# Kernel tuning notes

Measured on AMD Instinct MI355X. Metric: run time of the kernel, lower is better.

## Reference

```python
import jax, jax.numpy as jnp
import numpy as np

N = 50000       # nodes
E = 800000      # directed edges (before self-loops)
F_IN = 128      # dataset.num_features
HID = 16        # hidden per head (layer 1)
HEADS = 8
CLASSES = 16    # dataset.num_classes
NEG_SLOPE = 0.2 # GATConv default LeakyReLU slope


def setup_inputs() -> dict:
    key = jax.random.key(0)
    ks = jax.random.split(key, 10)
    s = 0.1  # glorot-ish scale for weights
    x = jax.random.normal(ks[0], (N, F_IN), jnp.float32)
    edge_index = jax.random.randint(ks[1], (2, E), 0, N, jnp.int32)
    W1 = jax.random.normal(ks[2], (F_IN, HEADS * HID), jnp.float32) * s
    a_src1 = jax.random.normal(ks[3], (HEADS, HID), jnp.float32) * s
    a_dst1 = jax.random.normal(ks[4], (HEADS, HID), jnp.float32) * s
    b1 = jnp.zeros((HEADS * HID,), jnp.float32)
    W2 = jax.random.normal(ks[5], (HEADS * HID, CLASSES), jnp.float32) * s
    a_src2 = jax.random.normal(ks[6], (1, CLASSES), jnp.float32) * s
    a_dst2 = jax.random.normal(ks[7], (1, CLASSES), jnp.float32) * s
    b2 = jnp.zeros((CLASSES,), jnp.float32)
    return {"x": x, "edge_index": edge_index, "W1": W1, "a_src1": a_src1,
            "a_dst1": a_dst1, "b1": b1, "W2": W2, "a_src2": a_src2,
            "a_dst2": a_dst2, "b2": b2}


def gat_conv(x, src, dst, W, a_s, a_d, b, concat):
    """PyG GATConv (eval mode): linear -> per-edge LeakyReLU attention ->
    per-destination segment softmax -> scatter-add aggregation."""
    n = x.shape[0]
    H, C = a_s.shape
    h = (x @ W).reshape(n, H, C)                       # [N,H,C]
    alpha_src = jnp.einsum('nhc,hc->nh', h, a_s)       # [N,H]
    alpha_dst = jnp.einsum('nhc,hc->nh', h, a_d)
    e = jax.nn.leaky_relu(alpha_src[src] + alpha_dst[dst], NEG_SLOPE)  # [E,H]
    # numerically stable segment softmax over incoming edges of each dst node
    emax = jax.ops.segment_max(e, dst, num_segments=n)
    emax = jnp.where(jnp.isfinite(emax), emax, 0.0)
    ex = jnp.exp(e - emax[dst])
    denom = jax.ops.segment_sum(ex, dst, num_segments=n)
    alpha = ex / (denom[dst] + 1e-16)                  # [E,H]
    out = jax.ops.segment_sum(alpha[:, :, None] * h[src], dst, num_segments=n)
    out = out.reshape(n, H * C) if concat else out.mean(axis=1)
    return out + b


def reference(x, edge_index, W1, a_src1, a_dst1, b1, W2, a_src2, a_dst2, b2):
    n = x.shape[0]
    loop = jnp.arange(n, dtype=edge_index.dtype)       # GATConv add_self_loops=True
    src = jnp.concatenate([edge_index[0], loop])
    dst = jnp.concatenate([edge_index[1], loop])
    # dropout layers are identity in eval mode
    h = jax.nn.elu(gat_conv(x, src, dst, W1, a_src1, a_dst1, b1, concat=True))
    out = gat_conv(h, src, dst, W2, a_src2, a_dst2, b2, concat=False)
    return out
```

## Files before the change

kernel.cpp:

```cpp
#include <hip/hip_runtime.h>
#include <hip/hip_bf16.h>
#include <math.h>

#define NN 50000
#define NE 800000
#define NBK 196
#define BCAP 5120
#define CHUNK 8192
#define NCH ((NE + CHUNK - 1) / CHUNK)
#define APITCH 136

typedef short bf16x8 __attribute__((ext_vector_type(8)));
typedef float f32x4  __attribute__((ext_vector_type(4)));
typedef float f32x2  __attribute__((ext_vector_type(2)));

__device__ __forceinline__ unsigned short f2bf(float f) {
    union { float f; unsigned int i; } v; v.f = f;
    unsigned int x = v.i;
    unsigned int r = (x >> 16) & 1u;
    x += 0x7fffu + r;
    return (unsigned short)(x >> 16);
}
__device__ __forceinline__ void un2(unsigned int u, float& a, float& b) {
    union { unsigned int i; float f; } x, y;
    x.i = u << 16; y.i = u & 0xffff0000u;
    a = x.f; b = y.f;
}
__device__ __forceinline__ f32x2 up2(unsigned int u) {
    union { unsigned int i; float f; } x, y;
    x.i = u << 16; y.i = u & 0xffff0000u;
    return (f32x2){x.f, y.f};
}

__global__ __launch_bounds__(256) void k_bin(const int* __restrict__ ei,
                                             int* __restrict__ gcur,
                                             unsigned int* __restrict__ packed) {
    __shared__ int h[NBK];
    __shared__ int bas[NBK];
    int t = threadIdx.x;
    if (t < NBK) h[t] = 0;
    __syncthreads();
    int cb = blockIdx.x * CHUNK;
#pragma unroll
    for (int k = 0; k < CHUNK / 256; k++) {
        int i = cb + k * 256 + t;
        if (i < NE) atomicAdd(&h[ei[NE + i] >> 8], 1);
    }
    __syncthreads();
    if (t < NBK) {
        int c = h[t];
        bas[t] = c ? (t * BCAP + atomicAdd(&gcur[t], c)) : 0;
        h[t] = 0;
    }
    __syncthreads();
#pragma unroll
    for (int k = 0; k < CHUNK / 256; k++) {
        int i = cb + k * 256 + t;
        if (i < NE) {
            int s = ei[i], d = ei[NE + i];
            int b = d >> 8;
            int r = atomicAdd(&h[b], 1);
            packed[bas[b] + r] = (unsigned int)s | ((unsigned int)(d & 255) << 16);
        }
    }
}

__global__ __launch_bounds__(256) void k_final(const unsigned int* __restrict__ packed,
                                               const int* __restrict__ gcur,
                                               int* __restrict__ deg,
                                               int* __restrict__ offs,
                                               int* __restrict__ ssrc) {
    __shared__ unsigned int pk[BCAP + 64];
    __shared__ int osl[BCAP + 64];
    __shared__ int cnt[256], pre[256], cur[256];
    int t = threadIdx.x, b = blockIdx.x;
    int start = b * BCAP;
    int n = gcur[b];
    for (int i = t; i < n; i += 256) pk[i] = packed[start + i];
    cnt[t] = 0;
    __syncthreads();
    for (int i = t; i < n; i += 256) atomicAdd(&cnt[(pk[i] >> 16) & 255], 1);
    __syncthreads();
    int v = cnt[t];
    pre[t] = v;
    __syncthreads();
    for (int off = 1; off < 256; off <<= 1) {
        int u = (t >= off) ? pre[t - off] : 0;
        __syncthreads();
        pre[t] += u;
        __syncthreads();
    }
    int excl = pre[t] - v;
    int dst = b * 256 + t;
    if (dst < NN) { deg[dst] = v; offs[dst] = start + excl; }
    cur[t] = excl;
    __syncthreads();
    for (int i = t; i < n; i += 256) {
        unsigned int p = pk[i];
        int r = atomicAdd(&cur[(p >> 16) & 255], 1);
        osl[r] = (int)(p & 0xffffu);
    }
    __syncthreads();
    for (int i = t; i < n; i += 256) ssrc[start + i] = osl[i];
}

__global__ __launch_bounds__(256) void k_swizw(const float* __restrict__ W1,
                                               uint4* __restrict__ W1s) {
    int f = blockIdx.x * 256 + threadIdx.x;
    int nt = f >> 8, kc = (f >> 6) & 3, l = f & 63;
    int n  = nt * 16 + (l & 15);
    int k0 = kc * 32 + (l >> 4) * 8;
    unsigned int p[4];
#pragma unroll
    for (int jj = 0; jj < 4; jj++) {
        float v0 = W1[(k0 + 2 * jj) * 128 + n];
        float v1 = W1[(k0 + 2 * jj + 1) * 128 + n];
        p[jj] = (unsigned int)f2bf(v0) | ((unsigned int)f2bf(v1) << 16);
    }
    W1s[f] = make_uint4(p[0], p[1], p[2], p[3]);
}

__global__ __launch_bounds__(256) void k_gemm1(
    const float* __restrict__ x,
    const uint4* __restrict__ W1s,
    const float* __restrict__ aS,
    const float* __restrict__ aD,
    unsigned short* __restrict__ h1,
    float* __restrict__ as1,
    float* __restrict__ ad1)
{
    __shared__ unsigned short Alds[64 * APITCH];
    int t = threadIdx.x;
    int w = t >> 6, l = t & 63;
    int rowbase = blockIdx.x * 64;

    {
        const float4* xg = (const float4*)(x + (size_t)rowbase * 128);
#pragma unroll
        for (int i = 0; i < 8; i++) {
            int idx = t + 256 * i;
            int r = idx >> 5, c = (idx & 31) * 4;
            float4 v = make_float4(0.f, 0.f, 0.f, 0.f);
            if (rowbase + r < NN) v = xg[idx];
            unsigned int p0 = (unsigned int)f2bf(v.x) | ((unsigned int)f2bf(v.y) << 16);
            unsigned int p1 = (unsigned int)f2bf(v.z) | ((unsigned int)f2bf(v.w) << 16);
            *(uint2*)&Alds[r * APITCH + c] = make_uint2(p0, p1);
        }
    }

    union BU { uint4 u; bf16x8 v; };
    BU b[2][4];
#pragma unroll
    for (int j = 0; j < 2; j++) {
        int nt = 2 * w + j;
#pragma unroll
        for (int kc = 0; kc < 4; kc++)
            b[j][kc].u = W1s[(nt * 4 + kc) * 64 + l];
    }
    __syncthreads();

    f32x4 acc[4][2];
#pragma unroll
    for (int mt = 0; mt < 4; mt++)
#pragma unroll
        for (int j = 0; j < 2; j++) acc[mt][j] = (f32x4){0.f, 0.f, 0.f, 0.f};

    int mrow = l & 15, quad = l >> 4;
#pragma unroll
    for (int kc = 0; kc < 4; kc++) {
#pragma unroll
        for (int mt = 0; mt < 4; mt++) {
            bf16x8 a = *(const bf16x8*)&Alds[(mt * 16 + mrow) * APITCH + kc * 32 + quad * 8];
            acc[mt][0] = __builtin_amdgcn_mfma_f32_16x16x32_bf16(a, b[0][kc].v, acc[mt][0], 0, 0, 0);
            acc[mt][1] = __builtin_amdgcn_mfma_f32_16x16x32_bf16(a, b[1][kc].v, acc[mt][1], 0, 0, 0);
        }
    }

#pragma unroll
    for (int j = 0; j < 2; j++) {
        int head = 2 * w + j;
        float aSv = aS[head * 16 + mrow];
        float aDv = aD[head * 16 + mrow];
#pragma unroll
        for (int mt = 0; mt < 4; mt++) {
#pragma unroll
            for (int reg = 0; reg < 4; reg++) {
                float s = acc[mt][j][reg] * aSv;
                float d = acc[mt][j][reg] * aDv;
                s += __shfl_xor(s, 1); s += __shfl_xor(s, 2);
                s += __shfl_xor(s, 4); s += __shfl_xor(s, 8);
                d += __shfl_xor(d, 1); d += __shfl_xor(d, 2);
                d += __shfl_xor(d, 4); d += __shfl_xor(d, 8);
                if (mrow == 0) {
                    int grow = rowbase + mt * 16 + quad * 4 + reg;
                    if (grow < NN) {
                        as1[grow * 8 + head] = s;
                        ad1[grow * 8 + head] = d;
                    }
                }
            }
        }
    }

    __syncthreads();
#pragma unroll
    for (int mt = 0; mt < 4; mt++)
#pragma unroll
        for (int j = 0; j < 2; j++) {
            int col = w * 32 + j * 16 + mrow;
#pragma unroll
            for (int reg = 0; reg < 4; reg++) {
                int r = mt * 16 + quad * 4 + reg;
                Alds[r * APITCH + col] = f2bf(acc[mt][j][reg]);
            }
        }
    __syncthreads();
    uint4* hg = (uint4*)h1;
#pragma unroll
    for (int i = 0; i < 4; i++) {
        int idx = t + 256 * i;
        int r = idx >> 4, ci = idx & 15;
        if (rowbase + r < NN)
            hg[(size_t)(rowbase + r) * 16 + ci] = *(const uint4*)&Alds[r * APITCH + ci * 8];
    }
}

__global__ __launch_bounds__(256) void k_agg1(
    const int* __restrict__ offs, const int* __restrict__ deg,
    const int* __restrict__ ssrc,
    const float* __restrict__ as1, const float* __restrict__ ad1,
    const unsigned short* __restrict__ h1, const float* __restrict__ b1,
    unsigned short* __restrict__ h2)
{
    int wave = threadIdx.x >> 6;
    int lane = threadIdx.x & 63;
    int node = blockIdx.x * 4 + wave;
    if (node >= NN) return;
    int start = offs[node], cnt = deg[node];

    int li = lane & 7, jg = lane >> 3;
    float adv = ad1[node * 8 + li];

    const uint4* h1u4 = (const uint4*)h1;
    f32x2 acc[8];
#pragma unroll
    for (int i = 0; i < 8; i++) acc[i] = (f32x2){0.f, 0.f};
    float dsum = 0.f;

    for (int base = 0; base <= cnt; base += 16) {
#pragma unroll
        for (int u = 0; u < 2; u++) {
            int j = base + u * 8 + jg;
            if (j <= cnt) {
                int s = (j < cnt) ? ssrc[start + j] : node;
                float e = as1[s * 8 + li] + adv;
                e = (e > 0.f) ? e : 0.2f * e;
                float w = __expf(e);
                uint4 ha = h1u4[(size_t)s * 16 + 2 * li];
                uint4 hb = h1u4[(size_t)s * 16 + 2 * li + 1];
                f32x2 w2 = (f32x2){w, w};
                acc[0] += w2 * up2(ha.x); acc[1] += w2 * up2(ha.y);
                acc[2] += w2 * up2(ha.z); acc[3] += w2 * up2(ha.w);
                acc[4] += w2 * up2(hb.x); acc[5] += w2 * up2(hb.y);
                acc[6] += w2 * up2(hb.z); acc[7] += w2 * up2(hb.w);
                dsum += w;
            }
        }
    }

#pragma unroll
    for (int i = 0; i < 8; i++) {
        acc[i].x += __shfl_xor(acc[i].x, 8);  acc[i].y += __shfl_xor(acc[i].y, 8);
        acc[i].x += __shfl_xor(acc[i].x, 16); acc[i].y += __shfl_xor(acc[i].y, 16);
        acc[i].x += __shfl_xor(acc[i].x, 32); acc[i].y += __shfl_xor(acc[i].y, 32);
    }
    dsum += __shfl_xor(dsum, 8);
    dsum += __shfl_xor(dsum, 16);
    dsum += __shfl_xor(dsum, 32);

    if (jg == 0) {
        float inv = 1.0f / dsum;
        int c0 = li * 16;
        float v[16];
#pragma unroll
        for (int i = 0; i < 8; i++) {
            float v0 = acc[i].x * inv + b1[c0 + 2 * i];
            float v1 = acc[i].y * inv + b1[c0 + 2 * i + 1];
            v[2 * i]     = (v0 > 0.f) ? v0 : (__expf(v0) - 1.0f);
            v[2 * i + 1] = (v1 > 0.f) ? v1 : (__expf(v1) - 1.0f);
        }
        uint4 o0, o1;
        o0.x = (unsigned int)f2bf(v[0])  | ((unsigned int)f2bf(v[1])  << 16);
        o0.y = (unsigned int)f2bf(v[2])  | ((unsigned int)f2bf(v[3])  << 16);
        o0.z = (unsigned int)f2bf(v[4])  | ((unsigned int)f2bf(v[5])  << 16);
        o0.w = (unsigned int)f2bf(v[6])  | ((unsigned int)f2bf(v[7])  << 16);
        o1.x = (unsigned int)f2bf(v[8])  | ((unsigned int)f2bf(v[9])  << 16);
        o1.y = (unsigned int)f2bf(v[10]) | ((unsigned int)f2bf(v[11]) << 16);
        o1.z = (unsigned int)f2bf(v[12]) | ((unsigned int)f2bf(v[13]) << 16);
        o1.w = (unsigned int)f2bf(v[14]) | ((unsigned int)f2bf(v[15]) << 16);
        ((uint4*)h2)[(size_t)node * 16 + 2 * li] = o0;
        ((uint4*)h2)[(size_t)node * 16 + 2 * li + 1] = o1;
    }
}

__global__ __launch_bounds__(256) void k_gemm2(
    const unsigned short* __restrict__ h2,
    const float* __restrict__ W2,
    const float* __restrict__ aS2,
    const float* __restrict__ aD2,
    float* __restrict__ g2,
    float* __restrict__ as2, float* __restrict__ ad2)
{
    __shared__ float Wl[128 * 16];
    __shared__ float xl[32 * 129];
    __shared__ float aSf[16], aDf[16];
    int t = threadIdx.x;

    for (int i = t; i < 2048; i += 256) Wl[i] = W2[i];
    if (t < 16) { aSf[t] = aS2[t]; aDf[t] = aD2[t]; }

    int rowbase = blockIdx.x * 32;
    for (int i = t; i < 2048; i += 256) {
        int row = rowbase + (i >> 6);
        unsigned int u = (row < NN) ? ((const unsigned int*)h2)[(size_t)rowbase * 64 + i] : 0u;
        float a, b; un2(u, a, b);
        int lin = 2 * i;
        int rr = lin >> 7, kk = lin & 127;
        xl[rr * 129 + kk] = a;
        xl[rr * 129 + kk + 1] = b;
    }
    __syncthreads();

    int r = t >> 3, cp = t & 7;
    int row = rowbase + r;
    float a0 = 0.f, a1 = 0.f;
    const float* xrow = &xl[r * 129];
#pragma unroll 4
    for (int k = 0; k < 128; k++) {
        float xv = xrow[k];
        a0 += xv * Wl[k * 16 + 2 * cp];
        a1 += xv * Wl[k * 16 + 2 * cp + 1];
    }
    if (row < NN) ((float2*)g2)[(size_t)row * 8 + cp] = make_float2(a0, a1);

    float asp = a0 * aSf[2 * cp] + a1 * aSf[2 * cp + 1];
    float adp = a0 * aDf[2 * cp] + a1 * aDf[2 * cp + 1];
    asp += __shfl_xor(asp, 1); asp += __shfl_xor(asp, 2); asp += __shfl_xor(asp, 4);
    adp += __shfl_xor(adp, 1); adp += __shfl_xor(adp, 2); adp += __shfl_xor(adp, 4);
    if (cp == 0 && row < NN) { as2[row] = asp; ad2[row] = adp; }
}

__global__ __launch_bounds__(256) void k_agg2(
    const int* __restrict__ offs, const int* __restrict__ deg,
    const int* __restrict__ ssrc,
    const float* __restrict__ as2, const float* __restrict__ ad2,
    const float* __restrict__ g2, const float* __restrict__ b2,
    float* __restrict__ out)
{
    int wave = threadIdx.x >> 6;
    int lane = threadIdx.x & 63;
    int node = blockIdx.x * 4 + wave;
    if (node >= NN) return;
    int start = offs[node], cnt = deg[node];
    float adv = ad2[node];

    int li4 = lane & 3, jg = lane >> 2;
    const float4* g2f4 = (const float4*)g2;

    float a0 = 0.f, a1 = 0.f, a2 = 0.f, a3 = 0.f, dsum = 0.f;
    for (int base = 0; base <= cnt; base += 16) {
        int j = base + jg;
        if (j <= cnt) {
            int s = (j < cnt) ? ssrc[start + j] : node;
            float e = as2[s] + adv;
            e = (e > 0.f) ? e : 0.2f * e;
            float w = __expf(e);
            float4 g = g2f4[(size_t)s * 4 + li4];
            a0 += w * g.x; a1 += w * g.y; a2 += w * g.z; a3 += w * g.w;
            if (li4 == 0) dsum += w;
        }
    }
#pragma unroll
    for (int m = 4; m < 64; m <<= 1) {
        a0 += __shfl_xor(a0, m); a1 += __shfl_xor(a1, m);
        a2 += __shfl_xor(a2, m); a3 += __shfl_xor(a3, m);
        dsum += __shfl_xor(dsum, m);
    }
    dsum += __shfl_xor(dsum, 1);
    dsum += __shfl_xor(dsum, 2);

    if (jg == 0) {
        float inv = 1.0f / dsum;
        const float4* b2f4 = (const float4*)b2;
        float4 bb = b2f4[li4];
        float4 o = make_float4(a0 * inv + bb.x, a1 * inv + bb.y,
                               a2 * inv + bb.z, a3 * inv + bb.w);
        ((float4*)out)[(size_t)node * 4 + li4] = o;
    }
}

extern "C" void kernel_launch(void* const* d_in, const int* in_sizes, int n_in,
                              void* d_out, int out_size, void* d_ws, size_t ws_size,
                              hipStream_t stream) {
    const float* x   = (const float*)d_in[0];
    const int*   ei  = (const int*)d_in[1];
    const float* W1  = (const float*)d_in[2];
    const float* aS1 = (const float*)d_in[3];
    const float* aD1 = (const float*)d_in[4];
    const float* b1  = (const float*)d_in[5];
    const float* W2  = (const float*)d_in[6];
    const float* aS2 = (const float*)d_in[7];
    const float* aD2 = (const float*)d_in[8];
    const float* b2  = (const float*)d_in[9];

    char* ws = (char*)d_ws;
    size_t off = 0;
    auto alloc = [&](size_t bytes) { void* p = ws + off; off += (bytes + 255) & ~(size_t)255; return p; };

    unsigned short* h1 = (unsigned short*)alloc((size_t)NN * 128 * 2);
    unsigned short* h2 = (unsigned short*)alloc((size_t)NN * 128 * 2);
    float* as1 = (float*)alloc((size_t)NN * 8 * 4);
    float* ad1 = (float*)alloc((size_t)NN * 8 * 4);
    float* g2  = (float*)alloc((size_t)NN * 16 * 4);
    float* as2 = (float*)alloc((size_t)NN * 4);
    float* ad2 = (float*)alloc((size_t)NN * 4);
    int* deg    = (int*)alloc((size_t)NN * 4);
    int* offs   = (int*)alloc((size_t)NN * 4);
    int* ssrc   = (int*)alloc((size_t)NBK * BCAP * 4);
    unsigned int* packed = (unsigned int*)alloc((size_t)NBK * BCAP * 4);
    int* gcur   = (int*)alloc((size_t)NBK * 4);
    uint4* W1s  = (uint4*)alloc((size_t)2048 * 16);

    hipMemsetAsync(gcur, 0, (size_t)NBK * 4, stream);
    k_bin<<<NCH, 256, 0, stream>>>(ei, gcur, packed);
    k_final<<<NBK, 256, 0, stream>>>(packed, gcur, deg, offs, ssrc);

    k_swizw<<<8, 256, 0, stream>>>(W1, W1s);
    k_gemm1<<<(NN + 63) / 64, 256, 0, stream>>>(x, W1s, aS1, aD1, h1, as1, ad1);
    k_agg1<<<(NN + 3) / 4, 256, 0, stream>>>(offs, deg, ssrc, as1, ad1, h1, b1, h2);
    k_gemm2<<<(NN + 31) / 32, 256, 0, stream>>>(h2, W2, aS2, aD2, g2, as2, ad2);
    k_agg2<<<(NN + 3) / 4, 256, 0, stream>>>(offs, deg, ssrc, as2, ad2, g2, b2,
                                             (float*)d_out);
}
```

Before: 217.9 us.

## Fuse edge binning into GEMM1 launch and unroll aggregation edge loops wider

The edge-binning kernel and the layer-1 GEMM now run as one launch: the first NCH blocks bin edges and the remaining blocks do the GEMM, with shared memory unioned between the two roles. The gcur reset moves from a memset into the weight-swizzle kernel. This removes a memset and two launches and lets the binning overlap with the GEMM. The agg1 and agg2 edge loops are also unrolled twice as wide to keep more gathers in flight per iteration, at the cost of more registers.

```diff
diff --git a/kernel.cpp b/kernel.cpp
--- a/kernel.cpp
+++ b/kernel.cpp
@@ -9,6 +9,7 @@
 #define CHUNK 8192
 #define NCH ((NE + CHUNK - 1) / CHUNK)
 #define APITCH 136
+#define G1BLOCKS ((NN + 63) / 64)
 
 typedef short bf16x8 __attribute__((ext_vector_type(8)));
 typedef float f32x4  __attribute__((ext_vector_type(4)));
@@ -32,81 +33,12 @@
     return (f32x2){x.f, y.f};
 }
 
-__global__ __launch_bounds__(256) void k_bin(const int* __restrict__ ei,
-                                             int* __restrict__ gcur,
-                                             unsigned int* __restrict__ packed) {
-    __shared__ int h[NBK];
-    __shared__ int bas[NBK];
+__global__ __launch_bounds__(256) void k_swizw(const float* __restrict__ W1,
+                                               uint4* __restrict__ W1s,
+                                               int* __restrict__ gcur) {
     int t = threadIdx.x;
-    if (t < NBK) h[t] = 0;
-    __syncthreads();
-    int cb = blockIdx.x * CHUNK;
-#pragma unroll
-    for (int k = 0; k < CHUNK / 256; k++) {
-        int i = cb + k * 256 + t;
-        if (i < NE) atomicAdd(&h[ei[NE + i] >> 8], 1);
-    }
-    __syncthreads();
-    if (t < NBK) {
-        int c = h[t];
-        bas[t] = c ? (t * BCAP + atomicAdd(&gcur[t], c)) : 0;
-        h[t] = 0;
-    }
-    __syncthreads();
-#pragma unroll
-    for (int k = 0; k < CHUNK / 256; k++) {
-        int i = cb + k * 256 + t;
-        if (i < NE) {
-            int s = ei[i], d = ei[NE + i];
-            int b = d >> 8;
-            int r = atomicAdd(&h[b], 1);
-            packed[bas[b] + r] = (unsigned int)s | ((unsigned int)(d & 255) << 16);
-        }
-    }
-}
-
-__global__ __launch_bounds__(256) void k_final(const unsigned int* __restrict__ packed,
-                                               const int* __restrict__ gcur,
-                                               int* __restrict__ deg,
-                                               int* __restrict__ offs,
-                                               int* __restrict__ ssrc) {
-    __shared__ unsigned int pk[BCAP + 64];
-    __shared__ int osl[BCAP + 64];
-    __shared__ int cnt[256], pre[256], cur[256];
-    int t = threadIdx.x, b = blockIdx.x;
-    int start = b * BCAP;
-    int n = gcur[b];
-    for (int i = t; i < n; i += 256) pk[i] = packed[start + i];
-    cnt[t] = 0;
-    __syncthreads();
-    for (int i = t; i < n; i += 256) atomicAdd(&cnt[(pk[i] >> 16) & 255], 1);
-    __syncthreads();
-    int v = cnt[t];
-    pre[t] = v;
-    __syncthreads();
-    for (int off = 1; off < 256; off <<= 1) {
-        int u = (t >= off) ? pre[t - off] : 0;
-        __syncthreads();
-        pre[t] += u;
-        __syncthreads();
-    }
-    int excl = pre[t] - v;
-    int dst = b * 256 + t;
-    if (dst < NN) { deg[dst] = v; offs[dst] = start + excl; }
-    cur[t] = excl;
-    __syncthreads();
-    for (int i = t; i < n; i += 256) {
-        unsigned int p = pk[i];
-        int r = atomicAdd(&cur[(p >> 16) & 255], 1);
-        osl[r] = (int)(p & 0xffffu);
-    }
-    __syncthreads();
-    for (int i = t; i < n; i += 256) ssrc[start + i] = osl[i];
-}
-
-__global__ __launch_bounds__(256) void k_swizw(const float* __restrict__ W1,
-                                               uint4* __restrict__ W1s) {
-    int f = blockIdx.x * 256 + threadIdx.x;
+    if (blockIdx.x == 0 && t < NBK) gcur[t] = 0;
+    int f = blockIdx.x * 256 + t;
     int nt = f >> 8, kc = (f >> 6) & 3, l = f & 63;
     int n  = nt * 16 + (l & 15);
     int k0 = kc * 32 + (l >> 4) * 8;
@@ -120,19 +52,54 @@
     W1s[f] = make_uint4(p[0], p[1], p[2], p[3]);
 }
 
-__global__ __launch_bounds__(256) void k_gemm1(
-    const float* __restrict__ x,
-    const uint4* __restrict__ W1s,
-    const float* __restrict__ aS,
-    const float* __restrict__ aD,
-    unsigned short* __restrict__ h1,
-    float* __restrict__ as1,
+__global__ __launch_bounds__(256) void k_bin_gemm1(
+    const int* __restrict__ ei, int* __restrict__ gcur,
+    unsigned int* __restrict__ packed,
+    const float* __restrict__ x, const uint4* __restrict__ W1s,
+    const float* __restrict__ aS, const float* __restrict__ aD,
+    unsigned short* __restrict__ h1, float* __restrict__ as1,
     float* __restrict__ ad1)
 {
-    __shared__ unsigned short Alds[64 * APITCH];
+    __shared__ union {
+        struct { int h[NBK]; int bas[NBK]; } bin;
+        unsigned short alds[64 * APITCH];
+    } sm;
     int t = threadIdx.x;
+
+    if (blockIdx.x < NCH) {
+        int* h = sm.bin.h;
+        int* bas = sm.bin.bas;
+        if (t < NBK) h[t] = 0;
+        __syncthreads();
+        int cb = blockIdx.x * CHUNK;
+#pragma unroll
+        for (int k = 0; k < CHUNK / 256; k++) {
+            int i = cb + k * 256 + t;
+            if (i < NE) atomicAdd(&h[ei[NE + i] >> 8], 1);
+        }
+        __syncthreads();
+        if (t < NBK) {
+            int c = h[t];
+            bas[t] = c ? (t * BCAP + atomicAdd(&gcur[t], c)) : 0;
+            h[t] = 0;
+        }
+        __syncthreads();
+#pragma unroll
+        for (int k = 0; k < CHUNK / 256; k++) {
+            int i = cb + k * 256 + t;
+            if (i < NE) {
+                int s = ei[i], d = ei[NE + i];
+                int b = d >> 8;
+                int r = atomicAdd(&h[b], 1);
+                packed[bas[b] + r] = (unsigned int)s | ((unsigned int)(d & 255) << 16);
+            }
+        }
+        return;
+    }
+
+    unsigned short* Alds = sm.alds;
     int w = t >> 6, l = t & 63;
-    int rowbase = blockIdx.x * 64;
+    int rowbase = (blockIdx.x - NCH) * 64;
 
     {
         const float4* xg = (const float4*)(x + (size_t)rowbase * 128);
@@ -225,6 +192,45 @@
     }
 }
 
+__global__ __launch_bounds__(256) void k_final(const unsigned int* __restrict__ packed,
+                                               const int* __restrict__ gcur,
+                                               int* __restrict__ deg,
+                                               int* __restrict__ offs,
+                                               int* __restrict__ ssrc) {
+    __shared__ unsigned int pk[BCAP + 64];
+    __shared__ int osl[BCAP + 64];
+    __shared__ int cnt[256], pre[256], cur[256];
+    int t = threadIdx.x, b = blockIdx.x;
+    int start = b * BCAP;
+    int n = gcur[b];
+    for (int i = t; i < n; i += 256) pk[i] = packed[start + i];
+    cnt[t] = 0;
+    __syncthreads();
+    for (int i = t; i < n; i += 256) atomicAdd(&cnt[(pk[i] >> 16) & 255], 1);
+    __syncthreads();
+    int v = cnt[t];
+    pre[t] = v;
+    __syncthreads();
+    for (int off = 1; off < 256; off <<= 1) {
+        int u = (t >= off) ? pre[t - off] : 0;
+        __syncthreads();
+        pre[t] += u;
+        __syncthreads();
+    }
+    int excl = pre[t] - v;
+    int dst = b * 256 + t;
+    if (dst < NN) { deg[dst] = v; offs[dst] = start + excl; }
+    cur[t] = excl;
+    __syncthreads();
+    for (int i = t; i < n; i += 256) {
+        unsigned int p = pk[i];
+        int r = atomicAdd(&cur[(p >> 16) & 255], 1);
+        osl[r] = (int)(p & 0xffffu);
+    }
+    __syncthreads();
+    for (int i = t; i < n; i += 256) ssrc[start + i] = osl[i];
+}
+
 __global__ __launch_bounds__(256) void k_agg1(
     const int* __restrict__ offs, const int* __restrict__ deg,
     const int* __restrict__ ssrc,
@@ -247,9 +253,9 @@
     for (int i = 0; i < 8; i++) acc[i] = (f32x2){0.f, 0.f};
     float dsum = 0.f;
 
-    for (int base = 0; base <= cnt; base += 16) {
-#pragma unroll
-        for (int u = 0; u < 2; u++) {
+    for (int base = 0; base <= cnt; base += 32) {
+#pragma unroll
+        for (int u = 0; u < 4; u++) {
             int j = base + u * 8 + jg;
             if (j <= cnt) {
                 int s = (j < cnt) ? ssrc[start + j] : node;
@@ -368,16 +374,19 @@
     const float4* g2f4 = (const float4*)g2;
 
     float a0 = 0.f, a1 = 0.f, a2 = 0.f, a3 = 0.f, dsum = 0.f;
-    for (int base = 0; base <= cnt; base += 16) {
-        int j = base + jg;
-        if (j <= cnt) {
-            int s = (j < cnt) ? ssrc[start + j] : node;
-            float e = as2[s] + adv;
-            e = (e > 0.f) ? e : 0.2f * e;
-            float w = __expf(e);
-            float4 g = g2f4[(size_t)s * 4 + li4];
-            a0 += w * g.x; a1 += w * g.y; a2 += w * g.z; a3 += w * g.w;
-            if (li4 == 0) dsum += w;
+    for (int base = 0; base <= cnt; base += 32) {
+#pragma unroll
+        for (int u = 0; u < 2; u++) {
+            int j = base + u * 16 + jg;
+            if (j <= cnt) {
+                int s = (j < cnt) ? ssrc[start + j] : node;
+                float e = as2[s] + adv;
+                e = (e > 0.f) ? e : 0.2f * e;
+                float w = __expf(e);
+                float4 g = g2f4[(size_t)s * 4 + li4];
+                a0 += w * g.x; a1 += w * g.y; a2 += w * g.z; a3 += w * g.w;
+                if (li4 == 0) dsum += w;
+            }
         }
     }
 #pragma unroll
@@ -431,12 +440,10 @@
     int* gcur   = (int*)alloc((size_t)NBK * 4);
     uint4* W1s  = (uint4*)alloc((size_t)2048 * 16);
 
-    hipMemsetAsync(gcur, 0, (size_t)NBK * 4, stream);
-    k_bin<<<NCH, 256, 0, stream>>>(ei, gcur, packed);
+    k_swizw<<<8, 256, 0, stream>>>(W1, W1s, gcur);
+    k_bin_gemm1<<<NCH + G1BLOCKS, 256, 0, stream>>>(ei, gcur, packed,
+                                                    x, W1s, aS1, aD1, h1, as1, ad1);
     k_final<<<NBK, 256, 0, stream>>>(packed, gcur, deg, offs, ssrc);
-
-    k_swizw<<<8, 256, 0, stream>>>(W1, W1s);
-    k_gemm1<<<(NN + 63) / 64, 256, 0, stream>>>(x, W1s, aS1, aD1, h1, as1, ad1);
     k_agg1<<<(NN + 3) / 4, 256, 0, stream>>>(offs, deg, ssrc, as1, ad1, h1, b1, h2);
     k_gemm2<<<(NN + 31) / 32, 256, 0, stream>>>(h2, W2, aS2, aD2, g2, as2, ad2);
     k_agg2<<<(NN + 3) / 4, 256, 0, stream>>>(offs, deg, ssrc, as2, ad2, g2, b2,
```

After: 199.2 us. -8.6%, faster.
